# Performance work log

Measured on AMD Instinct MI355X. Metric: run time of the kernel, lower is better.

The kernel has to match this reference:

```python
import jax, jax.numpy as jnp
import numpy as np

NEG_SLOPE = 0.01


def _pos(x):
    return jnp.where(x > 0, x, jnp.zeros_like(x))


def _neg(x):
    return jnp.where(x < 0, x, jnp.zeros_like(x))


def setup_inputs() -> dict:
    N = 4096
    key = jax.random.key(0)
    k1, k2, k3, k4, k5, k6 = jax.random.split(key, 6)
    x = jax.random.normal(k1, (1, N), dtype=jnp.float32)
    eps = 0.1
    lb0 = x - eps
    ub0 = x + eps
    scale = 1.0 / np.sqrt(N)
    W1 = jax.random.normal(k2, (N, N), dtype=jnp.float32) * scale
    b1 = jax.random.normal(k3, (1, N), dtype=jnp.float32)
    W2 = jax.random.normal(k4, (N, N), dtype=jnp.float32) * scale
    b2 = jax.random.normal(k5, (1, N), dtype=jnp.float32)
    raw_alpha = jax.random.normal(k6, (N,), dtype=jnp.float32)
    return {"lb0": lb0, "ub0": ub0, "W1": W1, "b1": b1, "W2": W2, "b2": b2, "raw_alpha": raw_alpha}


def reference(lb0, ub0, W1, b1, W2, b2, raw_alpha):
    N = raw_alpha.shape[0]
    ns = NEG_SLOPE
    # ---- backsubstitution: fold layer2 transformer through layer1 (affine: lslope=uslope=W1) ----
    clslope, clintercept, cuslope, cuintercept = W2, b2, W2, b2
    clp, cln = _pos(clslope), _neg(clslope)
    cup, cun = _pos(cuslope), _neg(cuslope)
    clintercept = b1 @ clp.T + b1 @ cln.T + clintercept  # [1,N]
    cuintercept = b1 @ cup.T + b1 @ cun.T + cuintercept
    clslope = clp @ W1 + cln @ W1  # [N,N]
    cuslope = cup @ W1 + cun @ W1
    # ---- certifier against initial interval bounds ----
    lsp, lsn = _pos(clslope), _neg(clslope)
    usp, usn = _pos(cuslope), _neg(cuslope)
    lbounds = lb0 @ lsp.T + ub0 @ lsn.T + clintercept  # [1,N]
    ubounds = ub0 @ usp.T + lb0 @ usn.T + cuintercept
    # ---- DeepPoly LeakyReLU relaxation (neg_slope <= 1 branch) ----
    alpha = jax.nn.sigmoid(raw_alpha)
    slope = ((ubounds - lbounds * ns) / (ubounds - lbounds)).reshape(-1)  # [N]
    slope = jnp.where(jnp.isnan(slope), jnp.zeros_like(slope), slope)
    intercept = (1.0 - slope) * ubounds  # [1,N]
    ones = jnp.ones((N,), dtype=lbounds.dtype)
    zeros_row = jnp.zeros((1, N), dtype=lbounds.dtype)
    lslope, lintercept = ones, zeros_row
    uslope, uintercept = ones, zeros_row
    below = (ubounds <= 0).reshape(-1)
    above = (lbounds >= 0).reshape(-1)
    lslope = jnp.where(below, ns * ones, lslope)
    uslope = jnp.where(below, ns * ones, uslope)
    lslope = jnp.where(above, ones, lslope)
    uslope = jnp.where(above, ones, uslope)
    crossing = ~(below | above)
    uslope = jnp.where(crossing, slope, uslope)
    uintercept = jnp.where(crossing, intercept, uintercept)
    lslope_v1 = jnp.where(crossing, ones, lslope)
    lslope_v2 = jnp.where(crossing, ns * ones, lslope)
    lslope = alpha * lslope_v1 + (1.0 - alpha) * lslope_v2
    return jnp.diag(lslope), lintercept, jnp.diag(uslope), uintercept
```

## Files before the change

kernel.cpp:

```cpp
#include <hip/hip_runtime.h>
#include <stdint.h>

#define NN 4096
#define NEG_SLOPE 0.01f

typedef _Float16 f16x8 __attribute__((ext_vector_type(8)));
typedef _Float16 f16x4 __attribute__((ext_vector_type(4)));
typedef float f32x4 __attribute__((ext_vector_type(4)));

__device__ __forceinline__ void async_ld16(void* lds, const void* g) {
    __builtin_amdgcn_global_load_lds(
        (__attribute__((address_space(1))) const void*)(const void*)g,
        (__attribute__((address_space(3))) void*)lds, 16, 0, 0);
}

__global__ __launch_bounds__(256, 4)
void gemm_bounds(const _Float16* __restrict__ Ah, const _Float16* __restrict__ Bt,
                 const float* __restrict__ lb0, const float* __restrict__ ub0,
                 float* __restrict__ lacc, float* __restrict__ uacc) {
    __shared__ _Float16 sA[128][32];
    __shared__ _Float16 sB[128][32];

    const int t = threadIdx.x;
    const int lane = t & 63;
    const int w = t >> 6;
    const int waveRow = w >> 1, waveCol = w & 1;
    const int quad = lane >> 4, l15 = lane & 15;

    const int bRow = (blockIdx.x >> 5) * 128;
    const int bCol = (blockIdx.x & 31) * 128;

    const int rIss = lane >> 2;
    const int cSwz = (lane & 3) ^ ((lane >> 3) & 3);
    const _Float16* gA = Ah + (size_t)(bRow + w * 32 + rIss) * NN + cSwz * 8;
    const _Float16* gB = Bt + (size_t)(bCol + w * 32 + rIss) * NN + cSwz * 8;

    f32x4 acc[4][4];
#pragma unroll
    for (int i = 0; i < 4; ++i)
#pragma unroll
        for (int j = 0; j < 4; ++j) acc[i][j] = (f32x4){0.f, 0.f, 0.f, 0.f};

    const int fswz = (l15 >> 1) & 3;

    for (int kt = 0; kt < NN / 32; ++kt) {
        const int k0 = kt * 32;
        __syncthreads();
        async_ld16(&sA[w * 32][0],      gA + k0);
        async_ld16(&sA[w * 32 + 16][0], gA + (size_t)16 * NN + k0);
        async_ld16(&sB[w * 32][0],      gB + k0);
        async_ld16(&sB[w * 32 + 16][0], gB + (size_t)16 * NN + k0);
        __syncthreads();

        f16x8 af[4];
#pragma unroll
        for (int fr = 0; fr < 4; ++fr) {
            const int r = waveRow * 64 + fr * 16 + l15;
            af[fr] = *(const f16x8*)&sA[r][(quad ^ fswz) * 8];
        }
#pragma unroll
        for (int fc = 0; fc < 4; ++fc) {
            const int c = waveCol * 64 + fc * 16 + l15;
            const f16x8 bf = *(const f16x8*)&sB[c][(quad ^ fswz) * 8];
#pragma unroll
            for (int fr = 0; fr < 4; ++fr)
                acc[fr][fc] = __builtin_amdgcn_mfma_f32_16x16x32_f16(af[fr], bf, acc[fr][fc], 0, 0, 0);
        }
    }

    float lbv[4], ubv[4];
#pragma unroll
    for (int fc = 0; fc < 4; ++fc) {
        const int col = bCol + waveCol * 64 + fc * 16 + l15;
        lbv[fc] = lb0[col];
        ubv[fc] = ub0[col];
    }
#pragma unroll
    for (int fr = 0; fr < 4; ++fr) {
#pragma unroll
        for (int r = 0; r < 4; ++r) {
            float ls = 0.f, us = 0.f;
#pragma unroll
            for (int fc = 0; fc < 4; ++fc) {
                const float m = acc[fr][fc][r];
                const float a = lbv[fc] * m, b = ubv[fc] * m;
                ls += fminf(a, b);
                us += fmaxf(a, b);
            }
#pragma unroll
            for (int mk = 1; mk < 16; mk <<= 1) {
                ls += __shfl_xor(ls, mk, 64);
                us += __shfl_xor(us, mk, 64);
            }
            if (l15 == 0) {
                const int row = bRow + waveRow * 64 + fr * 16 + quad * 4 + r;
                atomicAdd(&lacc[row], ls);
                atomicAdd(&uacc[row], us);
            }
        }
    }
}

__global__ __launch_bounds__(256)
void convertA(const float* __restrict__ W2, const float* __restrict__ b1,
              const float* __restrict__ b2, _Float16* __restrict__ Ah,
              float* __restrict__ cint) {
    const int j = blockIdx.x;
    const int t = threadIdx.x;
    const float* row = W2 + (size_t)j * NN;
    _Float16* orow = Ah + (size_t)j * NN;
    float dot = 0.f;
#pragma unroll
    for (int p = 0; p < 4; ++p) {
        const int i = t * 4 + p * 1024;
        const float4 v = *(const float4*)&row[i];
        const float4 bv = *(const float4*)&b1[i];
        dot += v.x * bv.x + v.y * bv.y + v.z * bv.z + v.w * bv.w;
        f16x4 h;
        h[0] = (_Float16)v.x; h[1] = (_Float16)v.y;
        h[2] = (_Float16)v.z; h[3] = (_Float16)v.w;
        *(f16x4*)&orow[i] = h;
    }
#pragma unroll
    for (int mk = 1; mk < 64; mk <<= 1) dot += __shfl_xor(dot, mk, 64);
    __shared__ float ws4[4];
    if ((t & 63) == 0) ws4[t >> 6] = dot;
    __syncthreads();
    if (t == 0) cint[j] = ws4[0] + ws4[1] + ws4[2] + ws4[3] + b2[j];
}

__global__ __launch_bounds__(256)
void convertB(const float* __restrict__ W1, _Float16* __restrict__ Bt) {
    __shared__ float sT[64][65];
    const int bk = (blockIdx.x & 63) * 64;
    const int bn = (blockIdx.x >> 6) * 64;
    const int t = threadIdx.x;
    const int r = t >> 4, c4 = (t & 15) * 4;
#pragma unroll
    for (int p = 0; p < 4; ++p) {
        const float4 v = *(const float4*)&W1[(size_t)(bk + r + p * 16) * NN + bn + c4];
        sT[r + p * 16][c4 + 0] = v.x;
        sT[r + p * 16][c4 + 1] = v.y;
        sT[r + p * 16][c4 + 2] = v.z;
        sT[r + p * 16][c4 + 3] = v.w;
    }
    __syncthreads();
    const int n = t >> 4, k4 = (t & 15) * 4;
#pragma unroll
    for (int p = 0; p < 4; ++p) {
        const int nn_ = n + p * 16;
        f16x4 h;
        h[0] = (_Float16)sT[k4 + 0][nn_];
        h[1] = (_Float16)sT[k4 + 1][nn_];
        h[2] = (_Float16)sT[k4 + 2][nn_];
        h[3] = (_Float16)sT[k4 + 3][nn_];
        *(f16x4*)&Bt[(size_t)(bn + nn_) * NN + bk + k4] = h;
    }
}

__global__ __launch_bounds__(256)
void clear_out(float4* __restrict__ out, size_t n4) {
    const size_t stride = (size_t)gridDim.x * 256;
    for (size_t p = (size_t)blockIdx.x * 256 + threadIdx.x; p < n4; p += stride)
        out[p] = make_float4(0.f, 0.f, 0.f, 0.f);
}

__global__ __launch_bounds__(256)
void final_kernel(const float* __restrict__ lacc, const float* __restrict__ uacc,
                  const float* __restrict__ cint, const float* __restrict__ ra,
                  float* __restrict__ out) {
    const int j = blockIdx.x * 256 + threadIdx.x;
    if (j >= NN) return;
    const float lb = lacc[j] + cint[j];
    const float ub = uacc[j] + cint[j];
    const float alpha = 1.f / (1.f + expf(-ra[j]));
    float s = (ub - lb * NEG_SLOPE) / (ub - lb);
    if (!(s == s)) s = 0.f;
    const float inter = (1.f - s) * ub;
    const bool below = (ub <= 0.f);
    const bool above = (lb >= 0.f);
    const bool crossing = !(below || above);
    const float uslope = crossing ? s : (below ? NEG_SLOPE : 1.f);
    const float uinter = crossing ? inter : 0.f;
    const float v1 = below ? NEG_SLOPE : 1.f;
    const float v2 = crossing ? NEG_SLOPE : (below ? NEG_SLOPE : 1.f);
    const float lslope = alpha * v1 + (1.f - alpha) * v2;

    const size_t N2 = (size_t)NN * NN;
    out[(size_t)j * NN + j] = lslope;
    out[N2 + NN + (size_t)j * NN + j] = uslope;
    out[2 * N2 + NN + j] = uinter;
}

extern "C" void kernel_launch(void* const* d_in, const int* in_sizes, int n_in,
                              void* d_out, int out_size, void* d_ws, size_t ws_size,
                              hipStream_t stream) {
    const float* lb0 = (const float*)d_in[0];
    const float* ub0 = (const float*)d_in[1];
    const float* W1  = (const float*)d_in[2];
    const float* b1  = (const float*)d_in[3];
    const float* W2  = (const float*)d_in[4];
    const float* b2  = (const float*)d_in[5];
    const float* ra  = (const float*)d_in[6];
    float* out = (float*)d_out;

    _Float16* Ahalf = (_Float16*)d_out;
    _Float16* Bt    = Ahalf + (size_t)NN * NN;

    float* lacc = (float*)d_ws;
    float* uacc = lacc + NN;
    float* cint = uacc + NN;

    hipMemsetAsync(d_ws, 0, 2 * NN * sizeof(float), stream);
    convertA<<<dim3(NN), dim3(256), 0, stream>>>(W2, b1, b2, Ahalf, cint);
    convertB<<<dim3(4096), dim3(256), 0, stream>>>(W1, Bt);
    gemm_bounds<<<dim3(1024), dim3(256), 0, stream>>>(Ahalf, Bt, lb0, ub0, lacc, uacc);
    clear_out<<<dim3(4096), dim3(256), 0, stream>>>((float4*)d_out, ((size_t)out_size) / 4);
    final_kernel<<<dim3(NN / 256), dim3(256), 0, stream>>>(lacc, uacc, cint, ra, out);
}
```

Before: 416.5 us.

## Use center-radius bound form, fuse output clearing into diagonal writer, widen K tile

Rewrites the interval bounds as center plus or minus radius. The center term W2·(W1·c) is computed exactly in fp32 through matrix-vector products fused into the prep kernels, and the GEMM epilogue only accumulates the radius term |M|·e. This halves the epilogue work and the atomics. The GEMM K tile doubles to 64 with an 8-way XOR swizzle, which halves the number of sync rounds. The separate full-output clear kernel is merged into a row writer that stores zeros and the diagonal value in one pass, removing one extra pass over the large output.

```diff
diff --git a/kernel.cpp b/kernel.cpp
--- a/kernel.cpp
+++ b/kernel.cpp
@@ -15,25 +15,24 @@
 }
 
 __global__ __launch_bounds__(256, 4)
-void gemm_bounds(const _Float16* __restrict__ Ah, const _Float16* __restrict__ Bt,
-                 const float* __restrict__ lb0, const float* __restrict__ ub0,
-                 float* __restrict__ lacc, float* __restrict__ uacc) {
-    __shared__ _Float16 sA[128][32];
-    __shared__ _Float16 sB[128][32];
-
+void gemm_S(const _Float16* __restrict__ Ah, const _Float16* __restrict__ Bt,
+            const float* __restrict__ lb0, const float* __restrict__ ub0,
+            float* __restrict__ S) {
+    __shared__ _Float16 sA[128][64];
+    __shared__ _Float16 sB[128][64];
     const int t = threadIdx.x;
     const int lane = t & 63;
     const int w = t >> 6;
     const int waveRow = w >> 1, waveCol = w & 1;
-    const int quad = lane >> 4, l15 = lane & 15;
+    const int quad = lane >> 4, l15 = lane & 15, l7 = lane & 7;
 
     const int bRow = (blockIdx.x >> 5) * 128;
     const int bCol = (blockIdx.x & 31) * 128;
 
-    const int rIss = lane >> 2;
-    const int cSwz = (lane & 3) ^ ((lane >> 3) & 3);
-    const _Float16* gA = Ah + (size_t)(bRow + w * 32 + rIss) * NN + cSwz * 8;
-    const _Float16* gB = Bt + (size_t)(bCol + w * 32 + rIss) * NN + cSwz * 8;
+    const int rOff = lane >> 3;
+    const int uG   = (lane & 7) ^ (lane >> 3);
+    const _Float16* gA = Ah + (size_t)(bRow + w * 32 + rOff) * NN + uG * 8;
+    const _Float16* gB = Bt + (size_t)(bCol + w * 32 + rOff) * NN + uG * 8;
 
     f32x4 acc[4][4];
 #pragma unroll
@@ -41,108 +40,87 @@
 #pragma unroll
         for (int j = 0; j < 4; ++j) acc[i][j] = (f32x4){0.f, 0.f, 0.f, 0.f};
 
-    const int fswz = (l15 >> 1) & 3;
-
-    for (int kt = 0; kt < NN / 32; ++kt) {
-        const int k0 = kt * 32;
+    for (int kt = 0; kt < NN / 64; ++kt) {
+        const int k0 = kt * 64;
         __syncthreads();
-        async_ld16(&sA[w * 32][0],      gA + k0);
-        async_ld16(&sA[w * 32 + 16][0], gA + (size_t)16 * NN + k0);
-        async_ld16(&sB[w * 32][0],      gB + k0);
-        async_ld16(&sB[w * 32 + 16][0], gB + (size_t)16 * NN + k0);
+#pragma unroll
+        for (int i = 0; i < 4; ++i) {
+            async_ld16(&sA[w * 32 + i * 8][0], gA + (size_t)(i * 8) * NN + k0);
+            async_ld16(&sB[w * 32 + i * 8][0], gB + (size_t)(i * 8) * NN + k0);
+        }
         __syncthreads();
 
-        f16x8 af[4];
-#pragma unroll
-        for (int fr = 0; fr < 4; ++fr) {
-            const int r = waveRow * 64 + fr * 16 + l15;
-            af[fr] = *(const f16x8*)&sA[r][(quad ^ fswz) * 8];
-        }
-#pragma unroll
-        for (int fc = 0; fc < 4; ++fc) {
-            const int c = waveCol * 64 + fc * 16 + l15;
-            const f16x8 bf = *(const f16x8*)&sB[c][(quad ^ fswz) * 8];
-#pragma unroll
-            for (int fr = 0; fr < 4; ++fr)
-                acc[fr][fc] = __builtin_amdgcn_mfma_f32_16x16x32_f16(af[fr], bf, acc[fr][fc], 0, 0, 0);
-        }
-    }
-
-    float lbv[4], ubv[4];
+#pragma unroll
+        for (int s = 0; s < 2; ++s) {
+            f16x8 af[4];
+#pragma unroll
+            for (int fr = 0; fr < 4; ++fr) {
+                const int r = waveRow * 64 + fr * 16 + l15;
+                af[fr] = *(const f16x8*)&sA[r][((s * 4 + quad) ^ l7) * 8];
+            }
+#pragma unroll
+            for (int fc = 0; fc < 4; ++fc) {
+                const int c = waveCol * 64 + fc * 16 + l15;
+                const f16x8 bf = *(const f16x8*)&sB[c][((s * 4 + quad) ^ l7) * 8];
+#pragma unroll
+                for (int fr = 0; fr < 4; ++fr)
+                    acc[fr][fc] = __builtin_amdgcn_mfma_f32_16x16x32_f16(af[fr], bf, acc[fr][fc], 0, 0, 0);
+            }
+        }
+    }
+
+    float ev[4];
 #pragma unroll
     for (int fc = 0; fc < 4; ++fc) {
         const int col = bCol + waveCol * 64 + fc * 16 + l15;
-        lbv[fc] = lb0[col];
-        ubv[fc] = ub0[col];
+        ev[fc] = 0.5f * (ub0[col] - lb0[col]);
     }
 #pragma unroll
     for (int fr = 0; fr < 4; ++fr) {
 #pragma unroll
         for (int r = 0; r < 4; ++r) {
-            float ls = 0.f, us = 0.f;
-#pragma unroll
-            for (int fc = 0; fc < 4; ++fc) {
-                const float m = acc[fr][fc][r];
-                const float a = lbv[fc] * m, b = ubv[fc] * m;
-                ls += fminf(a, b);
-                us += fmaxf(a, b);
-            }
-#pragma unroll
-            for (int mk = 1; mk < 16; mk <<= 1) {
-                ls += __shfl_xor(ls, mk, 64);
-                us += __shfl_xor(us, mk, 64);
-            }
+            float sv = 0.f;
+#pragma unroll
+            for (int fc = 0; fc < 4; ++fc)
+                sv += ev[fc] * fabsf(acc[fr][fc][r]);
+#pragma unroll
+            for (int mk = 1; mk < 16; mk <<= 1)
+                sv += __shfl_xor(sv, mk, 64);
             if (l15 == 0) {
                 const int row = bRow + waveRow * 64 + fr * 16 + quad * 4 + r;
-                atomicAdd(&lacc[row], ls);
-                atomicAdd(&uacc[row], us);
+                atomicAdd(&S[row], sv);
             }
         }
     }
 }
 
 __global__ __launch_bounds__(256)
-void convertA(const float* __restrict__ W2, const float* __restrict__ b1,
-              const float* __restrict__ b2, _Float16* __restrict__ Ah,
-              float* __restrict__ cint) {
-    const int j = blockIdx.x;
-    const int t = threadIdx.x;
-    const float* row = W2 + (size_t)j * NN;
-    _Float16* orow = Ah + (size_t)j * NN;
-    float dot = 0.f;
+void prepB(const float* __restrict__ W1, const float* __restrict__ lb0,
+           const float* __restrict__ ub0, _Float16* __restrict__ Bt,
+           float* __restrict__ v) {
+    __shared__ float sT[64][65];
+    const int bi = (blockIdx.x & 63) * 64;
+    const int bn = (blockIdx.x >> 6) * 64;
+    const int t = threadIdx.x;
+    const int r = t >> 4, c4 = (t & 15) * 4;
+
+    const float4 lv = *(const float4*)&lb0[bn + c4];
+    const float4 uv = *(const float4*)&ub0[bn + c4];
+    const float cw0 = 0.5f * (lv.x + uv.x), cw1 = 0.5f * (lv.y + uv.y);
+    const float cw2 = 0.5f * (lv.z + uv.z), cw3 = 0.5f * (lv.w + uv.w);
+
 #pragma unroll
     for (int p = 0; p < 4; ++p) {
-        const int i = t * 4 + p * 1024;
-        const float4 v = *(const float4*)&row[i];
-        const float4 bv = *(const float4*)&b1[i];
-        dot += v.x * bv.x + v.y * bv.y + v.z * bv.z + v.w * bv.w;
-        f16x4 h;
-        h[0] = (_Float16)v.x; h[1] = (_Float16)v.y;
-        h[2] = (_Float16)v.z; h[3] = (_Float16)v.w;
-        *(f16x4*)&orow[i] = h;
-    }
-#pragma unroll
-    for (int mk = 1; mk < 64; mk <<= 1) dot += __shfl_xor(dot, mk, 64);
-    __shared__ float ws4[4];
-    if ((t & 63) == 0) ws4[t >> 6] = dot;
-    __syncthreads();
-    if (t == 0) cint[j] = ws4[0] + ws4[1] + ws4[2] + ws4[3] + b2[j];
-}
-
-__global__ __launch_bounds__(256)
-void convertB(const float* __restrict__ W1, _Float16* __restrict__ Bt) {
-    __shared__ float sT[64][65];
-    const int bk = (blockIdx.x & 63) * 64;
-    const int bn = (blockIdx.x >> 6) * 64;
-    const int t = threadIdx.x;
-    const int r = t >> 4, c4 = (t & 15) * 4;
-#pragma unroll
-    for (int p = 0; p < 4; ++p) {
-        const float4 v = *(const float4*)&W1[(size_t)(bk + r + p * 16) * NN + bn + c4];
-        sT[r + p * 16][c4 + 0] = v.x;
-        sT[r + p * 16][c4 + 1] = v.y;
-        sT[r + p * 16][c4 + 2] = v.z;
-        sT[r + p * 16][c4 + 3] = v.w;
+        const float4 a = *(const float4*)&W1[(size_t)(bi + r + p * 16) * NN + bn + c4];
+        sT[r + p * 16][c4 + 0] = a.x;
+        sT[r + p * 16][c4 + 1] = a.y;
+        sT[r + p * 16][c4 + 2] = a.z;
+        sT[r + p * 16][c4 + 3] = a.w;
+        float part = a.x * cw0 + a.y * cw1 + a.z * cw2 + a.w * cw3;
+#pragma unroll
+        for (int mk = 1; mk < 16; mk <<= 1)
+            part += __shfl_xor(part, mk, 64);
+        if ((t & 15) == 0) atomicAdd(&v[bi + r + p * 16], part);
     }
     __syncthreads();
     const int n = t >> 4, k4 = (t & 15) * 4;
@@ -154,42 +132,100 @@
         h[1] = (_Float16)sT[k4 + 1][nn_];
         h[2] = (_Float16)sT[k4 + 2][nn_];
         h[3] = (_Float16)sT[k4 + 3][nn_];
-        *(f16x4*)&Bt[(size_t)(bn + nn_) * NN + bk + k4] = h;
+        *(f16x4*)&Bt[(size_t)(bn + nn_) * NN + bi + k4] = h;
     }
 }
 
 __global__ __launch_bounds__(256)
-void clear_out(float4* __restrict__ out, size_t n4) {
-    const size_t stride = (size_t)gridDim.x * 256;
-    for (size_t p = (size_t)blockIdx.x * 256 + threadIdx.x; p < n4; p += stride)
-        out[p] = make_float4(0.f, 0.f, 0.f, 0.f);
+void prepA(const float* __restrict__ W2, const float* __restrict__ b1,
+           const float* __restrict__ b2, const float* __restrict__ v,
+           _Float16* __restrict__ Ah, float* __restrict__ u,
+           float* __restrict__ cj, float* __restrict__ S) {
+    const int j = blockIdx.x;
+    const int t = threadIdx.x;
+    const float* row = W2 + (size_t)j * NN;
+    _Float16* orow = Ah + (size_t)j * NN;
+    float d1 = 0.f, d2 = 0.f;
+#pragma unroll
+    for (int p = 0; p < 4; ++p) {
+        const int i = t * 4 + p * 1024;
+        const float4 a = *(const float4*)&row[i];
+        const float4 bb = *(const float4*)&b1[i];
+        const float4 vv = *(const float4*)&v[i];
+        d1 += a.x * bb.x + a.y * bb.y + a.z * bb.z + a.w * bb.w;
+        d2 += a.x * vv.x + a.y * vv.y + a.z * vv.z + a.w * vv.w;
+        f16x4 h;
+        h[0] = (_Float16)a.x; h[1] = (_Float16)a.y;
+        h[2] = (_Float16)a.z; h[3] = (_Float16)a.w;
+        *(f16x4*)&orow[i] = h;
+    }
+#pragma unroll
+    for (int mk = 1; mk < 64; mk <<= 1) {
+        d1 += __shfl_xor(d1, mk, 64);
+        d2 += __shfl_xor(d2, mk, 64);
+    }
+    __shared__ float w1s[4], w2s[4];
+    if ((t & 63) == 0) { w1s[t >> 6] = d1; w2s[t >> 6] = d2; }
+    __syncthreads();
+    if (t == 0) {
+        cj[j] = w1s[0] + w1s[1] + w1s[2] + w1s[3] + b2[j];
+        u[j]  = w2s[0] + w2s[1] + w2s[2] + w2s[3];
+        S[j]  = 0.f;
+    }
 }
 
 __global__ __launch_bounds__(256)
-void final_kernel(const float* __restrict__ lacc, const float* __restrict__ uacc,
-                  const float* __restrict__ cint, const float* __restrict__ ra,
-                  float* __restrict__ out) {
-    const int j = blockIdx.x * 256 + threadIdx.x;
-    if (j >= NN) return;
-    const float lb = lacc[j] + cint[j];
-    const float ub = uacc[j] + cint[j];
-    const float alpha = 1.f / (1.f + expf(-ra[j]));
-    float s = (ub - lb * NEG_SLOPE) / (ub - lb);
-    if (!(s == s)) s = 0.f;
-    const float inter = (1.f - s) * ub;
-    const bool below = (ub <= 0.f);
-    const bool above = (lb >= 0.f);
-    const bool crossing = !(below || above);
-    const float uslope = crossing ? s : (below ? NEG_SLOPE : 1.f);
-    const float uinter = crossing ? inter : 0.f;
-    const float v1 = below ? NEG_SLOPE : 1.f;
-    const float v2 = crossing ? NEG_SLOPE : (below ? NEG_SLOPE : 1.f);
-    const float lslope = alpha * v1 + (1.f - alpha) * v2;
-
+void write_out(const float* __restrict__ S, const float* __restrict__ u,
+               const float* __restrict__ cj, const float* __restrict__ ra,
+               float* __restrict__ out) {
     const size_t N2 = (size_t)NN * NN;
-    out[(size_t)j * NN + j] = lslope;
-    out[N2 + NN + (size_t)j * NN + j] = uslope;
-    out[2 * N2 + NN + j] = uinter;
+    const int b = blockIdx.x;
+    const int t = threadIdx.x;
+    if (b < 8192) {
+        const int j = b & 4095;
+        const bool isU = b >= 4096;
+        const float base = u[j] + cj[j];
+        const float Sv = S[j];
+        const float lb = base - Sv, ub = base + Sv;
+        const float alpha = 1.f / (1.f + expf(-ra[j]));
+        float s = (ub - lb * NEG_SLOPE) / (ub - lb);
+        if (!(s == s)) s = 0.f;
+        const bool below = (ub <= 0.f), above = (lb >= 0.f);
+        const bool crossing = !(below || above);
+        const float uslope = crossing ? s : (below ? NEG_SLOPE : 1.f);
+        const float v1 = below ? NEG_SLOPE : 1.f;
+        const float v2 = crossing ? NEG_SLOPE : v1;
+        const float lslope = alpha * v1 + (1.f - alpha) * v2;
+        const float dval = isU ? uslope : lslope;
+        float4* rowp = (float4*)(out + (isU ? (N2 + NN) : (size_t)0) + (size_t)j * NN);
+        const int dq = j >> 2, dr = j & 3;
+#pragma unroll
+        for (int q = 0; q < 4; ++q) {
+            const int i4 = t + q * 256;
+            float4 z = make_float4(0.f, 0.f, 0.f, 0.f);
+            if (i4 == dq) ((float*)&z)[dr] = dval;
+            rowp[i4] = z;
+        }
+    } else if (b == 8192) {
+        float4* rowp = (float4*)(out + N2);
+#pragma unroll
+        for (int q = 0; q < 4; ++q)
+            rowp[t + q * 256] = make_float4(0.f, 0.f, 0.f, 0.f);
+    } else {
+        float* rowp = out + 2 * N2 + NN;
+#pragma unroll
+        for (int q = 0; q < 16; ++q) {
+            const int j = t + q * 256;
+            const float base = u[j] + cj[j];
+            const float Sv = S[j];
+            const float lb = base - Sv, ub = base + Sv;
+            float s = (ub - lb * NEG_SLOPE) / (ub - lb);
+            if (!(s == s)) s = 0.f;
+            const bool below = (ub <= 0.f), above = (lb >= 0.f);
+            const bool crossing = !(below || above);
+            rowp[j] = crossing ? (1.f - s) * ub : 0.f;
+        }
+    }
 }
 
 extern "C" void kernel_launch(void* const* d_in, const int* in_sizes, int n_in,
@@ -207,14 +243,14 @@
     _Float16* Ahalf = (_Float16*)d_out;
     _Float16* Bt    = Ahalf + (size_t)NN * NN;
 
-    float* lacc = (float*)d_ws;
-    float* uacc = lacc + NN;
-    float* cint = uacc + NN;
-
-    hipMemsetAsync(d_ws, 0, 2 * NN * sizeof(float), stream);
-    convertA<<<dim3(NN), dim3(256), 0, stream>>>(W2, b1, b2, Ahalf, cint);
-    convertB<<<dim3(4096), dim3(256), 0, stream>>>(W1, Bt);
-    gemm_bounds<<<dim3(1024), dim3(256), 0, stream>>>(Ahalf, Bt, lb0, ub0, lacc, uacc);
-    clear_out<<<dim3(4096), dim3(256), 0, stream>>>((float4*)d_out, ((size_t)out_size) / 4);
-    final_kernel<<<dim3(NN / 256), dim3(256), 0, stream>>>(lacc, uacc, cint, ra, out);
-}
+    float* v  = (float*)d_ws;
+    float* S  = v + NN;
+    float* u  = S + NN;
+    float* cj = u + NN;
+
+    hipMemsetAsync(v, 0, NN * sizeof(float), stream);
+    prepB<<<dim3(4096), dim3(256), 0, stream>>>(W1, lb0, ub0, Bt, v);
+    prepA<<<dim3(NN), dim3(256), 0, stream>>>(W2, b1, b2, v, Ahalf, u, cj, S);
+    gemm_S<<<dim3(1024), dim3(256), 0, stream>>>(Ahalf, Bt, lb0, ub0, S);
+    write_out<<<dim3(8194), dim3(256), 0, stream>>>(S, u, cj, ra, out);
+}
```

New measurement: 398.3 us. 1.05x faster.
